# Kernel optimization log

Hardware: AMD Instinct MI355X
Metric: run time of the kernel (lower is better)

## Reference

```python
import jax, jax.numpy as jnp
import numpy as np

GROUPS = 32
EPS = 1e-5
NUM_HEADS = 8


def group_norm(x, gamma, beta):
    B, C, H, W = x.shape
    xg = x.reshape(B, GROUPS, C // GROUPS, H, W)
    mean = xg.mean(axis=(2, 3, 4), keepdims=True)
    var = xg.var(axis=(2, 3, 4), keepdims=True)
    xg = (xg - mean) * jax.lax.rsqrt(var + EPS)
    x = xg.reshape(B, C, H, W)
    return x * gamma[None, :, None, None] + beta[None, :, None, None]


def setup_inputs() -> dict:
    key = jax.random.key(0)
    k1, k2, k3 = jax.random.split(key, 3)
    C = 512
    x = jax.random.normal(k1, (16, C, 32, 32), dtype=jnp.float32)
    gn_gamma = jnp.ones((C,), dtype=jnp.float32)
    gn_beta = jnp.zeros((C,), dtype=jnp.float32)
    w_qkv = jax.random.normal(k2, (3 * C, C), dtype=jnp.float32) * 0.02
    b_qkv = jnp.zeros((3 * C,), dtype=jnp.float32)
    w_proj = jax.random.normal(k3, (C, C), dtype=jnp.float32) * 0.02
    b_proj = jnp.zeros((C,), dtype=jnp.float32)
    return {"x": x, "gn_gamma": gn_gamma, "gn_beta": gn_beta,
            "w_qkv": w_qkv, "b_qkv": b_qkv, "w_proj": w_proj, "b_proj": b_proj}


def reference(x, gn_gamma, gn_beta, w_qkv, b_qkv, w_proj, b_proj):
    B, C, H, W = x.shape
    nh = NUM_HEADS
    hd = C // nh
    h = group_norm(x, gn_gamma, gn_beta)
    # 1x1 conv == channel matmul: [B,3C,H,W]
    qkv = jnp.einsum('bchw,oc->bohw', h, w_qkv) + b_qkv[None, :, None, None]
    qkv = qkv.reshape(B, 3, nh, hd, H * W)
    q, k, v = qkv[:, 0], qkv[:, 1], qkv[:, 2]  # [B, nh, hd, HW]
    scale = hd ** -0.5
    # attn[b,n,i,j] = sum_d q[b,n,d,i] * k[b,n,d,j]
    attn = jax.nn.softmax(jnp.einsum('bndi,bndj->bnij', q, k) * scale, axis=-1)
    # h[b,n,d,i] = sum_j v[b,n,d,j] * attn[b,n,i,j]
    h = jnp.einsum('bndj,bnij->bndi', v, attn).reshape(B, C, H, W)
    out = jnp.einsum('bchw,oc->bohw', h, w_proj) + b_proj[None, :, None, None]
    return x + out
```

## Files before the change

kernel.cpp:

```cpp
#include <hip/hip_runtime.h>

typedef __bf16 bf16;
typedef __bf16 bf16x2 __attribute__((ext_vector_type(2)));
typedef __bf16 bf16x4 __attribute__((ext_vector_type(4)));
typedef __bf16 bf16x8 __attribute__((ext_vector_type(8)));
typedef float  f32x4  __attribute__((ext_vector_type(4)));
typedef float  f32x16 __attribute__((ext_vector_type(16)));
typedef unsigned int u32x4 __attribute__((ext_vector_type(4)));

#define MFMA32(a,b,c) __builtin_amdgcn_mfma_f32_32x32x16_bf16((a),(b),(c),0,0,0)

#if __has_builtin(__builtin_amdgcn_exp2f)
#define EXP2(x) __builtin_amdgcn_exp2f(x)
#else
#define EXP2(x) exp2f(x)
#endif

__device__ __forceinline__ void gll16(const void* g, void* l) {
  __builtin_amdgcn_global_load_lds((const __attribute__((address_space(1))) unsigned int*)g,
                                   (__attribute__((address_space(3))) unsigned int*)l, 16, 0, 0);
}

__device__ __forceinline__ unsigned pk2(float a, float b) {
  bf16x2 t = { (bf16)a, (bf16)b };
  return __builtin_bit_cast(unsigned, t);
}

__device__ __forceinline__ void pl32swap(unsigned &x, unsigned &y) {
  asm("v_permlane32_swap_b32 %0, %1" : "+v"(x), "+v"(y));
}

static constexpr int Cc = 512;
static constexpr int Ss = 1024;
#define QSCALE 0.18033688011112042f

__global__ __launch_bounds__(256) void k_wconv(const float* __restrict__ wq, const float* __restrict__ wp,
                                               bf16* __restrict__ wqb, bf16* __restrict__ wpb) {
  const int i = blockIdx.x * 256 + threadIdx.x;
  if (i * 4 < 786432) {
    float4 v = ((const float4*)wq)[i];
    bf16x4 o = { (bf16)v.x, (bf16)v.y, (bf16)v.z, (bf16)v.w };
    ((bf16x4*)wqb)[i] = o;
  } else {
    const int j = i - 786432 / 4;
    float4 v = ((const float4*)wp)[j];
    bf16x4 o = { (bf16)v.x, (bf16)v.y, (bf16)v.z, (bf16)v.w };
    ((bf16x4*)wpb)[j] = o;
  }
}

__global__ __launch_bounds__(256, 2) void k_gnorm(const float* __restrict__ x,
                                                  const float* __restrict__ gamma,
                                                  const float* __restrict__ beta,
                                                  bf16* __restrict__ ht) {
  const int g = blockIdx.x;
  const int b = blockIdx.y;
  const float* base = x + ((size_t)b * Cc + g * 16) * Ss;
  const int tid = threadIdx.x;

  f32x4 xr[16];
  float s = 0.f, sq = 0.f;
  #pragma unroll
  for (int k = 0; k < 16; ++k) {
    xr[k] = ((const f32x4*)base)[k * 256 + tid];
    s  += xr[k][0] + xr[k][1] + xr[k][2] + xr[k][3];
    sq += xr[k][0] * xr[k][0] + xr[k][1] * xr[k][1] + xr[k][2] * xr[k][2] + xr[k][3] * xr[k][3];
  }
  #pragma unroll
  for (int m = 1; m < 64; m <<= 1) { s += __shfl_xor(s, m); sq += __shfl_xor(sq, m); }
  __shared__ float red[8];
  if ((tid & 63) == 0) { red[tid >> 6] = s; red[4 + (tid >> 6)] = sq; }
  __syncthreads();
  const float stot = red[0] + red[1] + red[2] + red[3];
  const float sqt  = red[4] + red[5] + red[6] + red[7];
  const float mean = stot * (1.f / 16384.f);
  const float var  = sqt * (1.f / 16384.f) - mean * mean;
  const float rstd = rsqrtf(var + 1e-5f);

  float ga[16], bb[16];
  #pragma unroll
  for (int k = 0; k < 16; ++k) {
    ga[k] = gamma[g * 16 + k] * rstd;
    bb[k] = beta[g * 16 + k] - mean * ga[k];
  }

  bf16* dst0 = ht + ((size_t)b * Ss + tid * 4) * Cc + g * 16;
  #pragma unroll
  for (int j = 0; j < 4; ++j) {
    bf16x8 o0, o1;
    #pragma unroll
    for (int k = 0; k < 8; ++k)  o0[k] = (bf16)(xr[k][j] * ga[k] + bb[k]);
    #pragma unroll
    for (int k = 0; k < 8; ++k)  o1[k] = (bf16)(xr[8 + k][j] * ga[8 + k] + bb[8 + k]);
    bf16* d = dst0 + (size_t)j * Cc;
    *(bf16x8*)d = o0;
    *(bf16x8*)(d + 8) = o1;
  }
}

template<int MODE>
__global__ __launch_bounds__(256, 2) void k_gemm(const bf16* __restrict__ Aw,
                                                 const bf16* __restrict__ Bt,
                                                 const float* __restrict__ bias,
                                                 bf16* __restrict__ qo, bf16* __restrict__ ko,
                                                 bf16* __restrict__ vo,
                                                 const float* __restrict__ xres,
                                                 float* __restrict__ out) {
  const int nt = blockIdx.x, mt = blockIdx.y, b = blockIdx.z;
  const int M0 = mt * 128, N0 = nt * 128;
  __shared__ __align__(16) char lA[2][16384];
  __shared__ __align__(16) char lB[2][16384];
  const int tid = threadIdx.x;
  const int l = tid & 63, w = tid >> 6;
  const int wm = w >> 1, wn = w & 1;
  const int l31 = l & 31, h = l >> 5;
  const bf16* Bb = Bt + (size_t)b * Ss * Cc;

  const int r8 = tid >> 3, c8 = tid & 7;
  const int csw = (c8 ^ (r8 & 7)) * 16;
  const char* asrc = (const char*)Aw + (size_t)(M0 + r8) * 1024 + csw;
  const char* bsrc = (const char*)Bb + (size_t)(N0 + r8) * 1024 + csw;
  const int dstoff = tid * 16;

  f32x16 acc[2][2];
  #pragma unroll
  for (int i = 0; i < 2; ++i)
    #pragma unroll
    for (int j = 0; j < 2; ++j)
      #pragma unroll
      for (int r = 0; r < 16; ++r) acc[i][j][r] = 0.f;

  const int sw7 = l31 & 7;

  #pragma unroll
  for (int p = 0; p < 4; ++p)
    gll16(asrc + (size_t)p * 32768, (char*)lA[0] + dstoff + p * 4096);
  #pragma unroll
  for (int p = 0; p < 4; ++p)
    gll16(bsrc + (size_t)p * 32768, (char*)lB[0] + dstoff + p * 4096);

  #pragma unroll
  for (int kt = 0; kt < 8; ++kt) {
    const int cur = kt & 1;
    if (kt < 7) {
      #pragma unroll
      for (int p = 0; p < 4; ++p)
        gll16(asrc + (size_t)p * 32768 + (kt + 1) * 128, (char*)lA[cur ^ 1] + dstoff + p * 4096);
      #pragma unroll
      for (int p = 0; p < 4; ++p)
        gll16(bsrc + (size_t)p * 32768 + (kt + 1) * 128, (char*)lB[cur ^ 1] + dstoff + p * 4096);
      asm volatile("s_waitcnt vmcnt(8)" ::: "memory");
    } else {
      asm volatile("s_waitcnt vmcnt(0)" ::: "memory");
    }
    __builtin_amdgcn_s_barrier();
    __builtin_amdgcn_sched_barrier(0);

    __builtin_amdgcn_s_setprio(1);
    #pragma unroll
    for (int kb = 0; kb < 4; ++kb) {
      const int cA0 = ((kb * 2 + h) ^ sw7) * 16;
      const int rA0 = (wm * 2 + 0) * 32 + l31, rA1 = (wm * 2 + 1) * 32 + l31;
      const int rB0 = (wn * 2 + 0) * 32 + l31, rB1 = (wn * 2 + 1) * 32 + l31;
      bf16x8 a0 = *(const bf16x8*)((const char*)lA[cur] + rA0 * 128 + cA0);
      bf16x8 a1 = *(const bf16x8*)((const char*)lA[cur] + rA1 * 128 + cA0);
      bf16x8 b0 = *(const bf16x8*)((const char*)lB[cur] + rB0 * 128 + cA0);
      bf16x8 b1 = *(const bf16x8*)((const char*)lB[cur] + rB1 * 128 + cA0);
      acc[0][0] = MFMA32(a0, b0, acc[0][0]);
      acc[0][1] = MFMA32(a0, b1, acc[0][1]);
      acc[1][0] = MFMA32(a1, b0, acc[1][0]);
      acc[1][1] = MFMA32(a1, b1, acc[1][1]);
    }
    __builtin_amdgcn_s_setprio(0);
    if (kt < 7) {
      asm volatile("s_waitcnt lgkmcnt(0)" ::: "memory");
      __builtin_amdgcn_s_barrier();
    }
  }

  #pragma unroll
  for (int m = 0; m < 2; ++m) {
    const int ofr = M0 + wm * 64 + m * 32;
    #pragma unroll
    for (int n = 0; n < 2; ++n) {
      const int sI = N0 + wn * 64 + n * 32 + l31;
      #pragma unroll
      for (int Qi = 0; Qi < 4; ++Qi) {
        const int rb = Qi * 8 + h * 4;
        float v[4], bi[4];
        #pragma unroll
        for (int r = 0; r < 4; ++r) {
          v[r] = acc[m][n][Qi * 4 + r];
          bi[r] = bias[ofr + rb + r];
        }
        if (MODE == 0) {
          const int which = ofr >> 9;
          const int nh = (ofr >> 6) & 7;
          const int dbase = (ofr & 63) + rb;
          const size_t bh = (size_t)b * 8 + nh;
          if (which == 2) {
            #pragma unroll
            for (int r = 0; r < 4; ++r)
              vo[(bh * 64 + dbase + r) * 1024 + sI] = (bf16)(v[r] + bi[r]);
          } else {
            const float qs = which ? 1.f : QSCALE;
            bf16x4 pk = { (bf16)((v[0] + bi[0]) * qs), (bf16)((v[1] + bi[1]) * qs),
                          (bf16)((v[2] + bi[2]) * qs), (bf16)((v[3] + bi[3]) * qs) };
            bf16* dst = (which ? ko : qo) + (bh * 1024 + sI) * 64 + dbase;
            *(bf16x4*)dst = pk;
          }
        } else {
          #pragma unroll
          for (int r = 0; r < 4; ++r) {
            const size_t idx = ((size_t)b * 512 + ofr + rb + r) * 1024 + sI;
            out[idx] = xres[idx] + bi[r] + v[r];
          }
        }
      }
    }
  }
}

__global__ __launch_bounds__(256, 2) void k_attn(const bf16* __restrict__ qT,
                                                 const bf16* __restrict__ kT,
                                                 const bf16* __restrict__ vv,
                                                 bf16* __restrict__ ao) {
  const int it = blockIdx.x, nh = blockIdx.y, b = blockIdx.z;
  const size_t bh = (size_t)b * 8 + nh;
  const char* kh = (const char*)(kT + bh * 65536);
  const char* vh = (const char*)(vv + bh * 65536);
  __shared__ __align__(16) char smem[49152];
  const int tid = threadIdx.x;
  const int w = tid >> 6, l = tid & 63;
  const int l31 = l & 31, h = l >> 5;

  const bf16* qrow = qT + bh * 65536 + (size_t)(it * 256 + w * 64 + l31) * 64;
  bf16x8 qf[2][4];
  #pragma unroll
  for (int qb = 0; qb < 2; ++qb)
    #pragma unroll
    for (int kq = 0; kq < 4; ++kq)
      qf[qb][kq] = *(const bf16x8*)(qrow + qb * 2048 + kq * 16 + h * 8);

  const int c3 = tid >> 6;
  const int l31s = l & 31, hs = l >> 5;
  const char* ksrc = kh + (size_t)l31s * 128 + c3 * 32 + hs * 16;
  const char* vsrc = vh + (size_t)l31s * 2048 + c3 * 32 + hs * 16;
  char* lkd = smem + tid * 16;
  char* lvd = smem + 24576 + tid * 16;

  #pragma unroll
  for (int t0 = 0; t0 < 2; ++t0) {
    gll16(ksrc + (size_t)t0 * 8192,         lkd + t0 * 8192);
    gll16(ksrc + (size_t)t0 * 8192 + 4096,  lkd + t0 * 8192 + 4096);
    gll16(vsrc + (size_t)t0 * 128,          lvd + t0 * 8192);
    gll16(vsrc + (size_t)t0 * 128 + 65536,  lvd + t0 * 8192 + 4096);
  }

  f32x16 oacc[2][2];
  #pragma unroll
  for (int qb = 0; qb < 2; ++qb)
    #pragma unroll
    for (int dt = 0; dt < 2; ++dt)
      #pragma unroll
      for (int r = 0; r < 16; ++r) oacc[qb][dt][r] = 0.f;
  float lacc[2][2] = {{0.f, 0.f}, {0.f, 0.f}};

  int slot = 0;
  for (int t = 0; t < 16; ++t) {
    if (t < 15) asm volatile("s_waitcnt vmcnt(4)" ::: "memory");
    else        asm volatile("s_waitcnt vmcnt(0)" ::: "memory");
    __builtin_amdgcn_s_barrier();
    __builtin_amdgcn_sched_barrier(0);
    if (t <= 13) {
      const int sn = (slot == 0) ? 2 : slot - 1;
      gll16(ksrc + (size_t)(t + 2) * 8192,        lkd + sn * 8192);
      gll16(ksrc + (size_t)(t + 2) * 8192 + 4096, lkd + sn * 8192 + 4096);
      gll16(vsrc + (size_t)(t + 2) * 128,         lvd + sn * 8192);
      gll16(vsrc + (size_t)(t + 2) * 128 + 65536, lvd + sn * 8192 + 4096);
    }

    const char* lkc = smem + slot * 8192;
    const char* lvc = smem + 24576 + slot * 8192;

    bf16x8 pb[2][4];
    #pragma unroll
    for (int jt = 0; jt < 2; ++jt) {
      f32x16 sf[2];
      #pragma unroll
      for (int r = 0; r < 16; ++r) { sf[0][r] = 0.f; sf[1][r] = 0.f; }
      __builtin_amdgcn_s_setprio(1);
      #pragma unroll
      for (int kq = 0; kq < 4; ++kq) {
        bf16x8 a = *(const bf16x8*)(lkc + (jt * 4 + kq) * 1024 + l * 16);
        sf[0] = MFMA32(a, qf[0][kq], sf[0]);
        sf[1] = MFMA32(a, qf[1][kq], sf[1]);
      }
      __builtin_amdgcn_s_setprio(0);
      #pragma unroll
      for (int qb = 0; qb < 2; ++qb) {
        unsigned pw[4][2];
        #pragma unroll
        for (int Qi = 0; Qi < 4; ++Qi) {
          const float p0 = EXP2(sf[qb][Qi * 4 + 0]);
          const float p1 = EXP2(sf[qb][Qi * 4 + 1]);
          const float p2 = EXP2(sf[qb][Qi * 4 + 2]);
          const float p3 = EXP2(sf[qb][Qi * 4 + 3]);
          lacc[qb][0] += p0 + p1; lacc[qb][1] += p2 + p3;
          pw[Qi][0] = pk2(p0, p1);
          pw[Qi][1] = pk2(p2, p3);
        }
        #pragma unroll
        for (int sq = 0; sq < 2; ++sq) {
          unsigned x0 = pw[2 * sq][0], y0 = pw[2 * sq + 1][0];
          unsigned x1 = pw[2 * sq][1], y1 = pw[2 * sq + 1][1];
          pl32swap(x0, y0);
          pl32swap(x1, y1);
          u32x4 wv = { x0, x1, y0, y1 };
          pb[qb][jt * 2 + sq] = __builtin_bit_cast(bf16x8, wv);
        }
      }
    }

    __builtin_amdgcn_s_setprio(1);
    #pragma unroll
    for (int dt = 0; dt < 2; ++dt) {
      #pragma unroll
      for (int s = 0; s < 4; ++s) {
        bf16x8 av = *(const bf16x8*)(lvc + (dt * 4 + s) * 1024 + l * 16);
        oacc[0][dt] = MFMA32(av, pb[0][s], oacc[0][dt]);
        oacc[1][dt] = MFMA32(av, pb[1][s], oacc[1][dt]);
      }
    }
    __builtin_amdgcn_s_setprio(0);
    slot = (slot == 2) ? 0 : slot + 1;
  }

  #pragma unroll
  for (int qb = 0; qb < 2; ++qb) {
    float ls = lacc[qb][0] + lacc[qb][1];
    ls += __shfl_xor(ls, 32);
    const float rinv = 1.f / ls;
    bf16* aor = ao + ((size_t)b * 1024 + it * 256 + w * 64 + qb * 32 + l31) * 512 + nh * 64;
    #pragma unroll
    for (int dt = 0; dt < 2; ++dt) {
      #pragma unroll
      for (int Qi = 0; Qi < 4; ++Qi) {
        bf16x4 o = { (bf16)(oacc[qb][dt][Qi * 4 + 0] * rinv), (bf16)(oacc[qb][dt][Qi * 4 + 1] * rinv),
                     (bf16)(oacc[qb][dt][Qi * 4 + 2] * rinv), (bf16)(oacc[qb][dt][Qi * 4 + 3] * rinv) };
        *(bf16x4*)(aor + dt * 32 + Qi * 8 + h * 4) = o;
      }
    }
  }
}

extern "C" void kernel_launch(void* const* d_in, const int* in_sizes, int n_in,
                              void* d_out, int out_size, void* d_ws, size_t ws_size,
                              hipStream_t stream) {
  (void)in_sizes; (void)n_in; (void)out_size; (void)ws_size;
  const float* x   = (const float*)d_in[0];
  const float* gam = (const float*)d_in[1];
  const float* bet = (const float*)d_in[2];
  const float* wq  = (const float*)d_in[3];
  const float* bq  = (const float*)d_in[4];
  const float* wp  = (const float*)d_in[5];
  const float* bp  = (const float*)d_in[6];
  float* out = (float*)d_out;

  bf16* ws  = (bf16*)d_ws;
  bf16* ht  = ws;
  bf16* qT  = ws + 8388608;
  bf16* kT  = ws + 16777216;
  bf16* vv  = ws + 25165824;
  bf16* wqb = ws + 33554432;
  bf16* wpb = ws + 34340864;

  k_wconv<<<1024, 256, 0, stream>>>(wq, wp, wqb, wpb);
  k_gnorm<<<dim3(32, 16), 256, 0, stream>>>(x, gam, bet, ht);
  k_gemm<0><<<dim3(8, 12, 16), 256, 0, stream>>>(wqb, ht, bq, qT, kT, vv, nullptr, nullptr);
  k_attn<<<dim3(4, 8, 16), 256, 0, stream>>>(qT, kT, vv, ht);
  k_gemm<1><<<dim3(8, 4, 16), 256, 0, stream>>>(wpb, ht, bp, nullptr, nullptr, nullptr, x, out);
}
```

Baseline: 126.0 us.

## Software-pipeline attention: overlap PV of previous tile with QK of current

Restructures the attention loop so each step runs the QK^T MFMAs for tile t interleaved with the PV MFMAs for tile t-1, using double-buffered probability registers. The LDS ring grows from three to four slots so the previous V tile stays resident, and the loop is fully unrolled. The aim is to hide the exp/pack latency behind matrix work. In exchange it uses more LDS (64KB per block) and more registers, which could lower occupancy below two blocks per CU.

```diff
diff --git a/kernel.cpp b/kernel.cpp
--- a/kernel.cpp
+++ b/kernel.cpp
@@ -221,6 +221,73 @@
   }
 }
 
+template<int DO_PV>
+__device__ __forceinline__ void tile_step(const char* lkc, const char* lvp,
+                                          const bf16x8 (&qf)[2][4],
+                                          const bf16x8 (&pbPrev)[2][4], bf16x8 (&pbCur)[2][4],
+                                          float (&lacc)[2][2], f32x16 (&oacc)[2][2], int l) {
+  #pragma unroll
+  for (int jt = 0; jt < 2; ++jt) {
+    f32x16 sf[2];
+    #pragma unroll
+    for (int r = 0; r < 16; ++r) { sf[0][r] = 0.f; sf[1][r] = 0.f; }
+    __builtin_amdgcn_s_setprio(1);
+    #pragma unroll
+    for (int kq = 0; kq < 4; ++kq) {
+      bf16x8 a = *(const bf16x8*)(lkc + (jt * 4 + kq) * 1024 + l * 16);
+      sf[0] = MFMA32(a, qf[0][kq], sf[0]);
+      sf[1] = MFMA32(a, qf[1][kq], sf[1]);
+    }
+    if (DO_PV) {
+      #pragma unroll
+      for (int s = 0; s < 4; ++s) {
+        bf16x8 av = *(const bf16x8*)(lvp + (jt * 4 + s) * 1024 + l * 16);
+        oacc[0][jt] = MFMA32(av, pbPrev[0][s], oacc[0][jt]);
+        oacc[1][jt] = MFMA32(av, pbPrev[1][s], oacc[1][jt]);
+      }
+    }
+    __builtin_amdgcn_s_setprio(0);
+    #pragma unroll
+    for (int qb = 0; qb < 2; ++qb) {
+      unsigned pw[4][2];
+      #pragma unroll
+      for (int Qi = 0; Qi < 4; ++Qi) {
+        const float p0 = EXP2(sf[qb][Qi * 4 + 0]);
+        const float p1 = EXP2(sf[qb][Qi * 4 + 1]);
+        const float p2 = EXP2(sf[qb][Qi * 4 + 2]);
+        const float p3 = EXP2(sf[qb][Qi * 4 + 3]);
+        lacc[qb][0] += p0 + p1; lacc[qb][1] += p2 + p3;
+        pw[Qi][0] = pk2(p0, p1);
+        pw[Qi][1] = pk2(p2, p3);
+      }
+      #pragma unroll
+      for (int sq = 0; sq < 2; ++sq) {
+        unsigned x0 = pw[2 * sq][0], y0 = pw[2 * sq + 1][0];
+        unsigned x1 = pw[2 * sq][1], y1 = pw[2 * sq + 1][1];
+        pl32swap(x0, y0);
+        pl32swap(x1, y1);
+        u32x4 wv = { x0, x1, y0, y1 };
+        pbCur[qb][jt * 2 + sq] = __builtin_bit_cast(bf16x8, wv);
+      }
+    }
+  }
+}
+
+__device__ __forceinline__ void pv_final(const char* lvp, const bf16x8 (&pb)[2][4],
+                                         f32x16 (&oacc)[2][2], int l) {
+  __builtin_amdgcn_s_setprio(1);
+  #pragma unroll
+  for (int dt = 0; dt < 2; ++dt) {
+    #pragma unroll
+    for (int s = 0; s < 4; ++s) {
+      bf16x8 av = *(const bf16x8*)(lvp + (dt * 4 + s) * 1024 + l * 16);
+      oacc[0][dt] = MFMA32(av, pb[0][s], oacc[0][dt]);
+      oacc[1][dt] = MFMA32(av, pb[1][s], oacc[1][dt]);
+    }
+  }
+  __builtin_amdgcn_s_setprio(0);
+}
+
 __global__ __launch_bounds__(256, 2) void k_attn(const bf16* __restrict__ qT,
                                                  const bf16* __restrict__ kT,
                                                  const bf16* __restrict__ vv,
@@ -229,7 +296,7 @@
   const size_t bh = (size_t)b * 8 + nh;
   const char* kh = (const char*)(kT + bh * 65536);
   const char* vh = (const char*)(vv + bh * 65536);
-  __shared__ __align__(16) char smem[49152];
+  __shared__ __align__(16) char smem[65536];
   const int tid = threadIdx.x;
   const int w = tid >> 6, l = tid & 63;
   const int l31 = l & 31, h = l >> 5;
@@ -247,7 +314,7 @@
   const char* ksrc = kh + (size_t)l31s * 128 + c3 * 32 + hs * 16;
   const char* vsrc = vh + (size_t)l31s * 2048 + c3 * 32 + hs * 16;
   char* lkd = smem + tid * 16;
-  char* lvd = smem + 24576 + tid * 16;
+  char* lvd = smem + 32768 + tid * 16;
 
   #pragma unroll
   for (int t0 = 0; t0 < 2; ++t0) {
@@ -265,76 +332,31 @@
       #pragma unroll
       for (int r = 0; r < 16; ++r) oacc[qb][dt][r] = 0.f;
   float lacc[2][2] = {{0.f, 0.f}, {0.f, 0.f}};
-
-  int slot = 0;
+  bf16x8 pbA[2][4], pbB[2][4];
+
+  #pragma unroll
   for (int t = 0; t < 16; ++t) {
     if (t < 15) asm volatile("s_waitcnt vmcnt(4)" ::: "memory");
     else        asm volatile("s_waitcnt vmcnt(0)" ::: "memory");
     __builtin_amdgcn_s_barrier();
     __builtin_amdgcn_sched_barrier(0);
     if (t <= 13) {
-      const int sn = (slot == 0) ? 2 : slot - 1;
+      const int sn = (t + 2) & 3;
       gll16(ksrc + (size_t)(t + 2) * 8192,        lkd + sn * 8192);
       gll16(ksrc + (size_t)(t + 2) * 8192 + 4096, lkd + sn * 8192 + 4096);
       gll16(vsrc + (size_t)(t + 2) * 128,         lvd + sn * 8192);
       gll16(vsrc + (size_t)(t + 2) * 128 + 65536, lvd + sn * 8192 + 4096);
     }
-
-    const char* lkc = smem + slot * 8192;
-    const char* lvc = smem + 24576 + slot * 8192;
-
-    bf16x8 pb[2][4];
-    #pragma unroll
-    for (int jt = 0; jt < 2; ++jt) {
-      f32x16 sf[2];
-      #pragma unroll
-      for (int r = 0; r < 16; ++r) { sf[0][r] = 0.f; sf[1][r] = 0.f; }
-      __builtin_amdgcn_s_setprio(1);
-      #pragma unroll
-      for (int kq = 0; kq < 4; ++kq) {
-        bf16x8 a = *(const bf16x8*)(lkc + (jt * 4 + kq) * 1024 + l * 16);
-        sf[0] = MFMA32(a, qf[0][kq], sf[0]);
-        sf[1] = MFMA32(a, qf[1][kq], sf[1]);
-      }
-      __builtin_amdgcn_s_setprio(0);
-      #pragma unroll
-      for (int qb = 0; qb < 2; ++qb) {
-        unsigned pw[4][2];
-        #pragma unroll
-        for (int Qi = 0; Qi < 4; ++Qi) {
-          const float p0 = EXP2(sf[qb][Qi * 4 + 0]);
-          const float p1 = EXP2(sf[qb][Qi * 4 + 1]);
-          const float p2 = EXP2(sf[qb][Qi * 4 + 2]);
-          const float p3 = EXP2(sf[qb][Qi * 4 + 3]);
-          lacc[qb][0] += p0 + p1; lacc[qb][1] += p2 + p3;
-          pw[Qi][0] = pk2(p0, p1);
-          pw[Qi][1] = pk2(p2, p3);
-        }
-        #pragma unroll
-        for (int sq = 0; sq < 2; ++sq) {
-          unsigned x0 = pw[2 * sq][0], y0 = pw[2 * sq + 1][0];
-          unsigned x1 = pw[2 * sq][1], y1 = pw[2 * sq + 1][1];
-          pl32swap(x0, y0);
-          pl32swap(x1, y1);
-          u32x4 wv = { x0, x1, y0, y1 };
-          pb[qb][jt * 2 + sq] = __builtin_bit_cast(bf16x8, wv);
-        }
-      }
-    }
-
-    __builtin_amdgcn_s_setprio(1);
-    #pragma unroll
-    for (int dt = 0; dt < 2; ++dt) {
-      #pragma unroll
-      for (int s = 0; s < 4; ++s) {
-        bf16x8 av = *(const bf16x8*)(lvc + (dt * 4 + s) * 1024 + l * 16);
-        oacc[0][dt] = MFMA32(av, pb[0][s], oacc[0][dt]);
-        oacc[1][dt] = MFMA32(av, pb[1][s], oacc[1][dt]);
-      }
-    }
-    __builtin_amdgcn_s_setprio(0);
-    slot = (slot == 2) ? 0 : slot + 1;
-  }
+    const char* lkc = smem + (t & 3) * 8192;
+    const char* lvp = smem + 32768 + ((t + 3) & 3) * 8192;
+    if (t == 0)
+      tile_step<0>(lkc, lvp, qf, pbB, pbA, lacc, oacc, l);
+    else if (t & 1)
+      tile_step<1>(lkc, lvp, qf, pbA, pbB, lacc, oacc, l);
+    else
+      tile_step<1>(lkc, lvp, qf, pbB, pbA, lacc, oacc, l);
+  }
+  pv_final(smem + 32768 + 3 * 8192, pbB, oacc, l);
 
   #pragma unroll
   for (int qb = 0; qb < 2; ++qb) {
```

New measurement: 125.8 us. No clear change (-0.2%).
